# Optimization experiments

Measured on AMD Instinct MI355X. Metric: run time of the kernel, lower is better.

## Reference

```python
import jax, jax.numpy as jnp
import numpy as np

B, N, H, NH = 2, 48, 256, 8
DH = H // NH  # attention head size = 32


def setup_inputs() -> dict:
    key = jax.random.key(0)
    ks = jax.random.split(key, 12)
    s = 0.02
    return {
        "attention_mask": jnp.zeros((B, 1, N, N), jnp.float32),
        "structure_matrix_pair": jax.random.normal(ks[0], (B, N, N, H), jnp.float32),
        "structure_matrix_triplet": jax.random.normal(ks[1], (B, N, N, N, H), jnp.float32),
        # Linear weights stored [in, out] (x @ W + b == torch Linear with W.T)
        "Wq": jax.random.normal(ks[2], (H, H), jnp.float32) * s, "bq": jnp.zeros((H,), jnp.float32),
        "Wk": jax.random.normal(ks[3], (H, H), jnp.float32) * s, "bk": jnp.zeros((H,), jnp.float32),
        "Wv": jax.random.normal(ks[4], (H, H), jnp.float32) * s, "bv": jnp.zeros((H,), jnp.float32),
        "Wsq": jax.random.normal(ks[5], (H, DH), jnp.float32) * s, "bsq": jnp.zeros((DH,), jnp.float32),
        "Wsk": jax.random.normal(ks[6], (H, DH), jnp.float32) * s, "bsk": jnp.zeros((DH,), jnp.float32),
        "Wsv": jax.random.normal(ks[7], (H, DH), jnp.float32) * s, "bsv": jnp.zeros((DH,), jnp.float32),
    }


def reference(attention_mask, structure_matrix_pair, structure_matrix_triplet,
              Wq, bq, Wk, bk, Wv, bv, Wsq, bsq, Wsk, bsk, Wsv, bsv):
    def heads(x):  # [B,N,N,H] -> [B,NH,N,N,DH]
        return x.reshape(B, N, N, NH, DH).transpose(0, 3, 1, 2, 4)

    q = heads(structure_matrix_pair @ Wq + bq)[:, :, :, None, :, :]  # [B,h,N,1,N,dh]
    k = heads(structure_matrix_pair @ Wk + bk)[:, :, :, :, None, :]  # [B,h,N,N,1,dh]
    v = heads(structure_matrix_pair @ Wv + bv)[:, :, :, None, :, :]  # [B,h,N,1,N,dh]

    sq = (structure_matrix_triplet @ Wsq + bsq)[:, None]  # [B,1,N,N,N,dh]
    sk = (structure_matrix_triplet @ Wsk + bsk)[:, None]
    sv = (structure_matrix_triplet @ Wsv + bsv)[:, None]

    q = q + sq  # [B,h,N,N,N,dh]
    k = k + sk
    v = v + sv

    scores = jnp.sum(q * k, axis=-1) / np.sqrt(DH).astype(np.float32)  # [B,h,N,N,N]
    scores = scores + attention_mask[:, :, None, :, :]
    probs = jax.nn.softmax(scores, axis=-1)
    # dropout is identity in eval mode
    ctx = jnp.einsum('bhikj,bhikjd->bhikd', probs, v)  # sum over last N (j)
    # [B,h,N,N,dh] -> [B,N,N,h*dh]
    return ctx.transpose(0, 2, 3, 1, 4).reshape(B, N, N, NH * DH)
```

## Files before the change

kernel.cpp:

```cpp
#include <hip/hip_runtime.h>
#include <hip/hip_bf16.h>

#define B_ 2
#define N_ 48
#define H_ 256
#define NH_ 8
#define DH_ 32
#define SQS_LD 100

typedef __attribute__((ext_vector_type(8))) short bf16x8;
typedef __attribute__((ext_vector_type(4))) float f32x4;

__device__ __forceinline__ unsigned short f2bf(float f) {
  unsigned u = __float_as_uint(f);
  u += 0x7FFFu + ((u >> 16) & 1u);
  return (unsigned short)(u >> 16);
}

__device__ __forceinline__ bf16x8 cvt8(float4 x, float4 y) {
  union { unsigned u[4]; bf16x8 v; } o;
  asm("v_cvt_pk_bf16_f32 %0, %1, %2" : "=v"(o.u[0]) : "v"(x.x), "v"(x.y));
  asm("v_cvt_pk_bf16_f32 %0, %1, %2" : "=v"(o.u[1]) : "v"(x.z), "v"(x.w));
  asm("v_cvt_pk_bf16_f32 %0, %1, %2" : "=v"(o.u[2]) : "v"(y.x), "v"(y.y));
  asm("v_cvt_pk_bf16_f32 %0, %1, %2" : "=v"(o.u[3]) : "v"(y.z), "v"(y.w));
  return o.v;
}

__global__ void pack_kernel(const float* __restrict__ Wq, const float* __restrict__ Wk,
                            const float* __restrict__ Wv, const float* __restrict__ bq,
                            const float* __restrict__ bk, const float* __restrict__ bv,
                            const float* __restrict__ Wsq, const float* __restrict__ Wsk,
                            const float* __restrict__ Wsv, const float* __restrict__ bsq,
                            const float* __restrict__ bsk, const float* __restrict__ bsv,
                            unsigned short* __restrict__ wfrag_pair,
                            unsigned short* __restrict__ wfrag_main,
                            float* __restrict__ biascat, float* __restrict__ biasm) {
  int t = blockIdx.x * 256 + threadIdx.x;
  if (t < 196608) {
    int i8 = t & 7, lane = (t >> 3) & 63, kt = (t >> 9) & 7, nt = t >> 12;
    int k = kt * 32 + ((lane >> 4) << 3) + i8;
    int n = nt * 16 + (lane & 15);
    const float* W = (n < 256) ? Wq : (n < 512) ? Wk : Wv;
    wfrag_pair[t] = f2bf(W[k * 256 + (n & 255)]);
  } else if (t < 196608 + 24576) {
    int p = t - 196608;
    int i8 = p & 7, lane = (p >> 3) & 63, kt = (p >> 9) & 7, nt = p >> 12;
    int k = kt * 32 + ((lane >> 4) << 3) + i8;
    int n = nt * 16 + (lane & 15);
    const float* W = (n < 32) ? Wsq : (n < 64) ? Wsk : Wsv;
    wfrag_main[p] = f2bf(W[k * 32 + (n & 31)]);
  } else if (t < 196608 + 24576 + 768) {
    int p = t - 196608 - 24576;
    const float* bsrc = (p < 256) ? bq : (p < 512) ? bk : bv;
    biascat[p] = bsrc[p & 255];
  } else if (t < 196608 + 24576 + 768 + 96) {
    int p = t - 196608 - 24576 - 768;
    biasm[p] = (p < 32) ? bsq[p] : (p < 64) ? bsk[p - 32] : bsv[p - 64];
  }
}

__device__ __forceinline__ void stage48x256(const float* __restrict__ src, char* tAc, int tid) {
#pragma unroll
  for (int it = 0; it < 4; ++it) {
    int c = it * 384 + tid;
    const float4* g = reinterpret_cast<const float4*>(src) + (c << 1);
    float4 x = g[0];
    float4 y = g[1];
    int row = c >> 5;
    int off = (row << 9) + ((c & 31) << 4);
    off ^= (row & 7) << 4;
    *reinterpret_cast<bf16x8*>(tAc + off) = cvt8(x, y);
  }
}

__global__ __launch_bounds__(384, 3)
void pair_proj_kernel(const float* __restrict__ pair,
                      const unsigned short* __restrict__ wfrag_pair,
                      const float* __restrict__ biascat, float* __restrict__ proj) {
  __shared__ __align__(16) char tAc[48 * 256 * 2];
  int tid = threadIdx.x;
  int lane = tid & 63;
  int wave = tid >> 6;
  int gm = blockIdx.x >> 3;
  int gn = blockIdx.x & 7;

  stage48x256(pair + (size_t)gm * 12288, tAc, tid);

  bf16x8 wf[8];
  {
    const bf16x8* wp = reinterpret_cast<const bf16x8*>(wfrag_pair);
#pragma unroll
    for (int kt = 0; kt < 8; ++kt) wf[kt] = wp[((gn * 6 + wave) * 8 + kt) * 64 + lane];
  }
  __syncthreads();

  f32x4 acc[3];
#pragma unroll
  for (int mt = 0; mt < 3; ++mt) acc[mt] = (f32x4){0.f, 0.f, 0.f, 0.f};
#pragma unroll
  for (int kt = 0; kt < 8; ++kt) {
#pragma unroll
    for (int mt = 0; mt < 3; ++mt) {
      int row = mt * 16 + (lane & 15);
      int off = (row << 9) + (kt << 6) + ((lane >> 4) << 4);
      off ^= (row & 7) << 4;
      bf16x8 a = *reinterpret_cast<const bf16x8*>(tAc + off);
      acc[mt] = __builtin_amdgcn_mfma_f32_16x16x32_bf16(a, wf[kt], acc[mt], 0, 0, 0);
    }
  }

  int col = gn * 96 + wave * 16 + (lane & 15);
  float bias = biascat[col];
  int jb = (lane >> 4) * 4;
#pragma unroll
  for (int mt = 0; mt < 3; ++mt) {
#pragma unroll
    for (int rr = 0; rr < 4; ++rr) {
      int j = mt * 16 + jb + rr;
      proj[(size_t)(gm * 48 + j) * 768 + col] = acc[mt][rr] + bias;
    }
  }
}

__global__ __launch_bounds__(384, 6)
void e2e_fused(const float* __restrict__ mask, const float* __restrict__ trip,
               const float* __restrict__ proj, const unsigned short* __restrict__ wfragm,
               const float* __restrict__ biasm, float* __restrict__ out) {
  __shared__ __align__(16) char smem[48 * 256 * 2];
  __shared__ float khl[256];
  __shared__ float pbuf[8][48];
  char* tAc = smem;
  float* sqS = reinterpret_cast<float*>(smem);

  int tid = threadIdx.x;
  int lane = tid & 63;
  int wave = tid >> 6;

  int bid = blockIdx.x;
  int s = (bid & 7) * 576 + (bid >> 3);
  int g = s / 48;
  int k = s % 48;
  int b = g / 48;
  int rowbase = g * 48;

  stage48x256(trip + (size_t)s * 12288, tAc, tid);
  if (tid < 256) khl[tid] = proj[(size_t)s * 768 + 256 + tid];
  __syncthreads();

  const bf16x8* wp = reinterpret_cast<const bf16x8*>(wfragm);
  f32x4 acc[3];
#pragma unroll
  for (int mt = 0; mt < 3; ++mt) acc[mt] = (f32x4){0.f, 0.f, 0.f, 0.f};
#pragma unroll
  for (int kt = 0; kt < 8; ++kt) {
    bf16x8 w = wp[(wave * 8 + kt) * 64 + lane];
#pragma unroll
    for (int mt = 0; mt < 3; ++mt) {
      int row = mt * 16 + (lane & 15);
      int off = (row << 9) + (kt << 6) + ((lane >> 4) << 4);
      off ^= (row & 7) << 4;
      bf16x8 a = *reinterpret_cast<const bf16x8*>(tAc + off);
      acc[mt] = __builtin_amdgcn_mfma_f32_16x16x32_bf16(a, w, acc[mt], 0, 0, 0);
    }
  }
  __syncthreads();

  {
    int n = wave * 16 + (lane & 15);
    float bias = biasm[n];
    int jb = (lane >> 4) * 4;
#pragma unroll
    for (int mt = 0; mt < 3; ++mt) {
#pragma unroll
      for (int rr = 0; rr < 4; ++rr)
        sqS[(mt * 16 + jb + rr) * SQS_LD + n] = acc[mt][rr] + bias;
    }
  }
  __syncthreads();

  {
    int j = tid % 48, h = tid / 48;
    const float4* q4 = reinterpret_cast<const float4*>(proj + (size_t)(rowbase + j) * 768 + h * 32);
    const float4* sq4 = reinterpret_cast<const float4*>(sqS + j * SQS_LD);
    const float4* kh4 = reinterpret_cast<const float4*>(khl + h * 32);
    float sc = 0.f;
#pragma unroll
    for (int d4 = 0; d4 < 8; ++d4) {
      float4 q = q4[d4];
      float4 sq = sq4[d4];
      float4 sk = sq4[8 + d4];
      float4 kh = kh4[d4];
      sc += (q.x + sq.x) * (kh.x + sk.x);
      sc += (q.y + sq.y) * (kh.y + sk.y);
      sc += (q.z + sq.z) * (kh.z + sk.z);
      sc += (q.w + sq.w) * (kh.w + sk.w);
    }
    pbuf[h][j] = sc * 0.17677669529663687f + mask[b * 2304 + k * 48 + j];
  }
  __syncthreads();

  for (int h = wave; h < 8; h += 6) {
    float x = (lane < 48) ? pbuf[h][lane] : -INFINITY;
    float m = x;
#pragma unroll
    for (int off = 32; off; off >>= 1) m = fmaxf(m, __shfl_xor(m, off));
    float e = (lane < 48) ? __expf(x - m) : 0.f;
    float sum = e;
#pragma unroll
    for (int off = 32; off; off >>= 1) sum += __shfl_xor(sum, off);
    if (lane < 48) pbuf[h][lane] = e / sum;
  }
  __syncthreads();

  if (tid < 256) {
    int h = tid >> 5, d = tid & 31;
    const float* vbase = proj + (size_t)rowbase * 768 + 512 + tid;
    float a = 0.f;
#pragma unroll 8
    for (int j = 0; j < 48; ++j)
      a += pbuf[h][j] * (vbase[(size_t)j * 768] + sqS[j * SQS_LD + 64 + d]);
    out[(size_t)s * 256 + tid] = a;
  }
}

extern "C" void kernel_launch(void* const* d_in, const int* in_sizes, int n_in,
                              void* d_out, int out_size, void* d_ws, size_t ws_size,
                              hipStream_t stream) {
  const float* mask = (const float*)d_in[0];
  const float* pair = (const float*)d_in[1];
  const float* trip = (const float*)d_in[2];
  const float* Wq = (const float*)d_in[3];
  const float* bq = (const float*)d_in[4];
  const float* Wk = (const float*)d_in[5];
  const float* bk = (const float*)d_in[6];
  const float* Wv = (const float*)d_in[7];
  const float* bv = (const float*)d_in[8];
  const float* Wsq = (const float*)d_in[9];
  const float* bsq = (const float*)d_in[10];
  const float* Wsk = (const float*)d_in[11];
  const float* bsk = (const float*)d_in[12];
  const float* Wsv = (const float*)d_in[13];
  const float* bsv = (const float*)d_in[14];

  char* ws = (char*)d_ws;
  float* proj = (float*)ws;
  unsigned short* wfrag_pair = (unsigned short*)(ws + 14155776);
  unsigned short* wfrag_main = (unsigned short*)(ws + 14155776 + 393216);
  float* biascat = (float*)(ws + 14155776 + 393216 + 49152);
  float* biasm = (float*)(ws + 14155776 + 393216 + 49152 + 3072);

  pack_kernel<<<867, 256, 0, stream>>>(Wq, Wk, Wv, bq, bk, bv, Wsq, Wsk, Wsv,
                                       bsq, bsk, bsv,
                                       wfrag_pair, wfrag_main, biascat, biasm);
  pair_proj_kernel<<<768, 384, 0, stream>>>(pair, wfrag_pair, biascat, proj);
  e2e_fused<<<4608, 384, 0, stream>>>(mask, trip, proj, wfrag_main, biasm,
                                      (float*)d_out);
}
```

Before: 84.15 us.

## Fold weight packing into pair projection, store Q/V as bf16, split trip staging

Removes the separate pack kernel. The pair projection now loads and converts its weight fragments from the fp32 weights directly, and its gn==7 blocks pack the triplet weights and biases. Projection outputs are split into separate planes: Q and V in bf16, K in fp32. This cuts the bytes the main kernel reads for Q and V, at some precision cost. The main kernel also stages the triplet tile in two halves so the MFMAs on the first half can overlap the LDS writes of the second, and uses a lighter barrier with only an lgkm wait.

```diff
diff --git a/kernel.cpp b/kernel.cpp
--- a/kernel.cpp
+++ b/kernel.cpp
@@ -26,37 +26,10 @@
   return o.v;
 }
 
-__global__ void pack_kernel(const float* __restrict__ Wq, const float* __restrict__ Wk,
-                            const float* __restrict__ Wv, const float* __restrict__ bq,
-                            const float* __restrict__ bk, const float* __restrict__ bv,
-                            const float* __restrict__ Wsq, const float* __restrict__ Wsk,
-                            const float* __restrict__ Wsv, const float* __restrict__ bsq,
-                            const float* __restrict__ bsk, const float* __restrict__ bsv,
-                            unsigned short* __restrict__ wfrag_pair,
-                            unsigned short* __restrict__ wfrag_main,
-                            float* __restrict__ biascat, float* __restrict__ biasm) {
-  int t = blockIdx.x * 256 + threadIdx.x;
-  if (t < 196608) {
-    int i8 = t & 7, lane = (t >> 3) & 63, kt = (t >> 9) & 7, nt = t >> 12;
-    int k = kt * 32 + ((lane >> 4) << 3) + i8;
-    int n = nt * 16 + (lane & 15);
-    const float* W = (n < 256) ? Wq : (n < 512) ? Wk : Wv;
-    wfrag_pair[t] = f2bf(W[k * 256 + (n & 255)]);
-  } else if (t < 196608 + 24576) {
-    int p = t - 196608;
-    int i8 = p & 7, lane = (p >> 3) & 63, kt = (p >> 9) & 7, nt = p >> 12;
-    int k = kt * 32 + ((lane >> 4) << 3) + i8;
-    int n = nt * 16 + (lane & 15);
-    const float* W = (n < 32) ? Wsq : (n < 64) ? Wsk : Wsv;
-    wfrag_main[p] = f2bf(W[k * 32 + (n & 31)]);
-  } else if (t < 196608 + 24576 + 768) {
-    int p = t - 196608 - 24576;
-    const float* bsrc = (p < 256) ? bq : (p < 512) ? bk : bv;
-    biascat[p] = bsrc[p & 255];
-  } else if (t < 196608 + 24576 + 768 + 96) {
-    int p = t - 196608 - 24576 - 768;
-    biasm[p] = (p < 32) ? bsq[p] : (p < 64) ? bsk[p - 32] : bsv[p - 64];
-  }
+__device__ __forceinline__ void bar_lgkm() {
+  asm volatile("s_waitcnt lgkmcnt(0)" ::: "memory");
+  __builtin_amdgcn_s_barrier();
+  asm volatile("" ::: "memory");
 }
 
 __device__ __forceinline__ void stage48x256(const float* __restrict__ src, char* tAc, int tid) {
@@ -75,8 +48,15 @@
 
 __global__ __launch_bounds__(384, 3)
 void pair_proj_kernel(const float* __restrict__ pair,
-                      const unsigned short* __restrict__ wfrag_pair,
-                      const float* __restrict__ biascat, float* __restrict__ proj) {
+                      const float* __restrict__ Wq, const float* __restrict__ Wk,
+                      const float* __restrict__ Wv, const float* __restrict__ bq,
+                      const float* __restrict__ bk, const float* __restrict__ bv,
+                      const float* __restrict__ Wsq, const float* __restrict__ Wsk,
+                      const float* __restrict__ Wsv, const float* __restrict__ bsq,
+                      const float* __restrict__ bsk, const float* __restrict__ bsv,
+                      unsigned short* __restrict__ qplane, float* __restrict__ kplane,
+                      unsigned short* __restrict__ vplane,
+                      unsigned short* __restrict__ wfrag_main, float* __restrict__ biasm) {
   __shared__ __align__(16) char tAc[48 * 256 * 2];
   int tid = threadIdx.x;
   int lane = tid & 63;
@@ -86,11 +66,39 @@
 
   stage48x256(pair + (size_t)gm * 12288, tAc, tid);
 
+  int col = gn * 96 + wave * 16 + (lane & 15);
+  const float* Wsel = (col < 256) ? Wq : (col < 512) ? Wk : Wv;
+  const float* bsel = (col < 256) ? bq : (col < 512) ? bk : bv;
+  int cc = col & 255;
   bf16x8 wf[8];
-  {
-    const bf16x8* wp = reinterpret_cast<const bf16x8*>(wfrag_pair);
-#pragma unroll
-    for (int kt = 0; kt < 8; ++kt) wf[kt] = wp[((gn * 6 + wave) * 8 + kt) * 64 + lane];
+#pragma unroll
+  for (int kt = 0; kt < 8; ++kt) {
+    int kbase = kt * 32 + ((lane >> 4) << 3);
+    float4 w0, w1;
+    w0.x = Wsel[(kbase + 0) * 256 + cc];
+    w0.y = Wsel[(kbase + 1) * 256 + cc];
+    w0.z = Wsel[(kbase + 2) * 256 + cc];
+    w0.w = Wsel[(kbase + 3) * 256 + cc];
+    w1.x = Wsel[(kbase + 4) * 256 + cc];
+    w1.y = Wsel[(kbase + 5) * 256 + cc];
+    w1.z = Wsel[(kbase + 6) * 256 + cc];
+    w1.w = Wsel[(kbase + 7) * 256 + cc];
+    wf[kt] = cvt8(w0, w1);
+  }
+  float bias = bsel[cc];
+
+  if (gn == 7) {
+    if (tid < 256) {
+      int p = gm * 256 + tid;
+      int i8 = p & 7, l2 = (p >> 3) & 63, kt2 = (p >> 9) & 7, nt2 = p >> 12;
+      int k2 = kt2 * 32 + ((l2 >> 4) << 3) + i8;
+      int n2 = nt2 * 16 + (l2 & 15);
+      const float* W = (n2 < 32) ? Wsq : (n2 < 64) ? Wsk : Wsv;
+      wfrag_main[p] = f2bf(W[k2 * 32 + (n2 & 31)]);
+    } else if (gm == 0 && tid < 352) {
+      int p = tid - 256;
+      biasm[p] = (p < 32) ? bsq[p] : (p < 64) ? bsk[p - 32] : bsv[p - 64];
+    }
   }
   __syncthreads();
 
@@ -109,22 +117,26 @@
     }
   }
 
-  int col = gn * 96 + wave * 16 + (lane & 15);
-  float bias = biascat[col];
   int jb = (lane >> 4) * 4;
 #pragma unroll
   for (int mt = 0; mt < 3; ++mt) {
 #pragma unroll
     for (int rr = 0; rr < 4; ++rr) {
       int j = mt * 16 + jb + rr;
-      proj[(size_t)(gm * 48 + j) * 768 + col] = acc[mt][rr] + bias;
+      size_t row = (size_t)(gm * 48 + j) * 256;
+      float val = acc[mt][rr] + bias;
+      if (col < 256) qplane[row + col] = f2bf(val);
+      else if (col < 512) kplane[row + (col - 256)] = val;
+      else vplane[row + (col - 512)] = f2bf(val);
     }
   }
 }
 
 __global__ __launch_bounds__(384, 6)
 void e2e_fused(const float* __restrict__ mask, const float* __restrict__ trip,
-               const float* __restrict__ proj, const unsigned short* __restrict__ wfragm,
+               const unsigned short* __restrict__ qplane, const float* __restrict__ kplane,
+               const unsigned short* __restrict__ vplane,
+               const unsigned short* __restrict__ wfragm,
                const float* __restrict__ biasm, float* __restrict__ out) {
   __shared__ __align__(16) char smem[48 * 256 * 2];
   __shared__ float khl[256];
@@ -143,16 +155,37 @@
   int b = g / 48;
   int rowbase = g * 48;
 
-  stage48x256(trip + (size_t)s * 12288, tAc, tid);
-  if (tid < 256) khl[tid] = proj[(size_t)s * 768 + 256 + tid];
-  __syncthreads();
+  if (tid < 256) khl[tid] = kplane[(size_t)s * 256 + tid];
+
+  const float4* src = reinterpret_cast<const float4*>(trip + (size_t)s * 12288);
+  int r0 = tid >> 4, c0 = tid & 15;
+  int r1 = (384 + tid) >> 4, c1 = tid & 15;
+  float4 pa[4], pb[4];
+  pa[0] = src[r0 * 64 + c0 * 2];
+  pa[1] = src[r0 * 64 + c0 * 2 + 1];
+  pa[2] = src[r1 * 64 + c1 * 2];
+  pa[3] = src[r1 * 64 + c1 * 2 + 1];
+  pb[0] = src[r0 * 64 + 32 + c0 * 2];
+  pb[1] = src[r0 * 64 + 32 + c0 * 2 + 1];
+  pb[2] = src[r1 * 64 + 32 + c1 * 2];
+  pb[3] = src[r1 * 64 + 32 + c1 * 2 + 1];
+
+  {
+    int off0 = (r0 << 9) + (c0 << 4);
+    off0 ^= (r0 & 7) << 4;
+    *reinterpret_cast<bf16x8*>(tAc + off0) = cvt8(pa[0], pa[1]);
+    int off1 = (r1 << 9) + (c1 << 4);
+    off1 ^= (r1 & 7) << 4;
+    *reinterpret_cast<bf16x8*>(tAc + off1) = cvt8(pa[2], pa[3]);
+  }
+  bar_lgkm();
 
   const bf16x8* wp = reinterpret_cast<const bf16x8*>(wfragm);
   f32x4 acc[3];
 #pragma unroll
   for (int mt = 0; mt < 3; ++mt) acc[mt] = (f32x4){0.f, 0.f, 0.f, 0.f};
 #pragma unroll
-  for (int kt = 0; kt < 8; ++kt) {
+  for (int kt = 0; kt < 4; ++kt) {
     bf16x8 w = wp[(wave * 8 + kt) * 64 + lane];
 #pragma unroll
     for (int mt = 0; mt < 3; ++mt) {
@@ -163,7 +196,29 @@
       acc[mt] = __builtin_amdgcn_mfma_f32_16x16x32_bf16(a, w, acc[mt], 0, 0, 0);
     }
   }
-  __syncthreads();
+  {
+    int off0 = (r0 << 9) + ((16 + c0) << 4);
+    off0 ^= (r0 & 7) << 4;
+    *reinterpret_cast<bf16x8*>(tAc + off0) = cvt8(pb[0], pb[1]);
+    int off1 = (r1 << 9) + ((16 + c1) << 4);
+    off1 ^= (r1 & 7) << 4;
+    *reinterpret_cast<bf16x8*>(tAc + off1) = cvt8(pb[2], pb[3]);
+  }
+  bar_lgkm();
+
+#pragma unroll
+  for (int kt = 4; kt < 8; ++kt) {
+    bf16x8 w = wp[(wave * 8 + kt) * 64 + lane];
+#pragma unroll
+    for (int mt = 0; mt < 3; ++mt) {
+      int row = mt * 16 + (lane & 15);
+      int off = (row << 9) + (kt << 6) + ((lane >> 4) << 4);
+      off ^= (row & 7) << 4;
+      bf16x8 a = *reinterpret_cast<const bf16x8*>(tAc + off);
+      acc[mt] = __builtin_amdgcn_mfma_f32_16x16x32_bf16(a, w, acc[mt], 0, 0, 0);
+    }
+  }
+  bar_lgkm();
 
   {
     int n = wave * 16 + (lane & 15);
@@ -176,28 +231,32 @@
         sqS[(mt * 16 + jb + rr) * SQS_LD + n] = acc[mt][rr] + bias;
     }
   }
-  __syncthreads();
+  bar_lgkm();
 
   {
     int j = tid % 48, h = tid / 48;
-    const float4* q4 = reinterpret_cast<const float4*>(proj + (size_t)(rowbase + j) * 768 + h * 32);
+    const uint4* qp = reinterpret_cast<const uint4*>(qplane + (size_t)(rowbase + j) * 256 + h * 32);
     const float4* sq4 = reinterpret_cast<const float4*>(sqS + j * SQS_LD);
     const float4* kh4 = reinterpret_cast<const float4*>(khl + h * 32);
     float sc = 0.f;
 #pragma unroll
-    for (int d4 = 0; d4 < 8; ++d4) {
-      float4 q = q4[d4];
-      float4 sq = sq4[d4];
-      float4 sk = sq4[8 + d4];
-      float4 kh = kh4[d4];
-      sc += (q.x + sq.x) * (kh.x + sk.x);
-      sc += (q.y + sq.y) * (kh.y + sk.y);
-      sc += (q.z + sq.z) * (kh.z + sk.z);
-      sc += (q.w + sq.w) * (kh.w + sk.w);
+    for (int q4i = 0; q4i < 4; ++q4i) {
+      uint4 qw = qp[q4i];
+      float4 sqA = sq4[q4i * 2], sqB = sq4[q4i * 2 + 1];
+      float4 skA = sq4[8 + q4i * 2], skB = sq4[8 + q4i * 2 + 1];
+      float4 khA = kh4[q4i * 2], khB = kh4[q4i * 2 + 1];
+      sc += (__uint_as_float(qw.x << 16) + sqA.x) * (khA.x + skA.x);
+      sc += (__uint_as_float(qw.x & 0xFFFF0000u) + sqA.y) * (khA.y + skA.y);
+      sc += (__uint_as_float(qw.y << 16) + sqA.z) * (khA.z + skA.z);
+      sc += (__uint_as_float(qw.y & 0xFFFF0000u) + sqA.w) * (khA.w + skA.w);
+      sc += (__uint_as_float(qw.z << 16) + sqB.x) * (khB.x + skB.x);
+      sc += (__uint_as_float(qw.z & 0xFFFF0000u) + sqB.y) * (khB.y + skB.y);
+      sc += (__uint_as_float(qw.w << 16) + sqB.z) * (khB.z + skB.z);
+      sc += (__uint_as_float(qw.w & 0xFFFF0000u) + sqB.w) * (khB.w + skB.w);
     }
     pbuf[h][j] = sc * 0.17677669529663687f + mask[b * 2304 + k * 48 + j];
   }
-  __syncthreads();
+  bar_lgkm();
 
   for (int h = wave; h < 8; h += 6) {
     float x = (lane < 48) ? pbuf[h][lane] : -INFINITY;
@@ -210,15 +269,17 @@
     for (int off = 32; off; off >>= 1) sum += __shfl_xor(sum, off);
     if (lane < 48) pbuf[h][lane] = e / sum;
   }
-  __syncthreads();
+  bar_lgkm();
 
   if (tid < 256) {
     int h = tid >> 5, d = tid & 31;
-    const float* vbase = proj + (size_t)rowbase * 768 + 512 + tid;
+    const unsigned short* vbase = vplane + (size_t)rowbase * 256 + tid;
     float a = 0.f;
 #pragma unroll 8
-    for (int j = 0; j < 48; ++j)
-      a += pbuf[h][j] * (vbase[(size_t)j * 768] + sqS[j * SQS_LD + 64 + d]);
+    for (int j = 0; j < 48; ++j) {
+      float v = __uint_as_float((unsigned)vbase[(size_t)j * 256] << 16);
+      a += pbuf[h][j] * (v + sqS[j * SQS_LD + 64 + d]);
+    }
     out[(size_t)s * 256 + tid] = a;
   }
 }
@@ -243,16 +304,16 @@
   const float* bsv = (const float*)d_in[14];
 
   char* ws = (char*)d_ws;
-  float* proj = (float*)ws;
-  unsigned short* wfrag_pair = (unsigned short*)(ws + 14155776);
-  unsigned short* wfrag_main = (unsigned short*)(ws + 14155776 + 393216);
-  float* biascat = (float*)(ws + 14155776 + 393216 + 49152);
-  float* biasm = (float*)(ws + 14155776 + 393216 + 49152 + 3072);
-
-  pack_kernel<<<867, 256, 0, stream>>>(Wq, Wk, Wv, bq, bk, bv, Wsq, Wsk, Wsv,
-                                       bsq, bsk, bsv,
-                                       wfrag_pair, wfrag_main, biascat, biasm);
-  pair_proj_kernel<<<768, 384, 0, stream>>>(pair, wfrag_pair, biascat, proj);
-  e2e_fused<<<4608, 384, 0, stream>>>(mask, trip, proj, wfrag_main, biasm,
-                                      (float*)d_out);
-}
+  unsigned short* qplane = (unsigned short*)ws;
+  float* kplane = (float*)(ws + 2359296);
+  unsigned short* vplane = (unsigned short*)(ws + 7077888);
+  unsigned short* wfrag_main = (unsigned short*)(ws + 9437184);
+  float* biasm = (float*)(ws + 9486336);
+
+  pair_proj_kernel<<<768, 384, 0, stream>>>(pair, Wq, Wk, Wv, bq, bk, bv,
+                                            Wsq, Wsk, Wsv, bsq, bsk, bsv,
+                                            qplane, kplane, vplane,
+                                            wfrag_main, biasm);
+  e2e_fused<<<4608, 384, 0, stream>>>(mask, trip, qplane, kplane, vplane,
+                                      wfrag_main, biasm, (float*)d_out);
+}
```

Measured after the change: 72.48 us. -13.9%, faster.
